# Kernel tuning notes

Hardware: AMD Instinct MI355X
Metric: run time of the kernel (lower is better)

## Reference

```python
import jax, jax.numpy as jnp
import numpy as np


def _conv(x, w, b):
    # PyTorch Conv2d(k=4, s=2, p=1): NCHW x OIHW correlation
    y = jax.lax.conv_general_dilated(x, w, window_strides=(2, 2),
                                     padding=((1, 1), (1, 1)),
                                     dimension_numbers=('NCHW', 'OIHW', 'NCHW'))
    return y + b[None, :, None, None]


def _conv_t(x, w, b):
    # PyTorch ConvTranspose2d(k=4, s=2, p=1); w has torch shape (Cin, Cout, 4, 4).
    # Adjoint of strided correlation = correlation with spatially-flipped,
    # channel-swapped kernel and lhs dilation; pad = k - 1 - p = 2.
    wk = jnp.flip(w, (2, 3)).transpose(1, 0, 2, 3)  # (Cout, Cin, 4, 4)
    y = jax.lax.conv_general_dilated(x, wk, window_strides=(1, 1),
                                     padding=((2, 2), (2, 2)),
                                     lhs_dilation=(2, 2),
                                     dimension_numbers=('NCHW', 'OIHW', 'NCHW'))
    return y + b[None, :, None, None]


def setup_inputs() -> dict:
    key = jax.random.key(0)
    ks = jax.random.split(key, 18)
    s = 0.05
    inp = {'x': jax.random.normal(ks[0], (32, 3, 256, 256), jnp.float32)}
    # encoder weights (OIHW)
    enc_shapes = [(64, 3, 4, 4), (128, 64, 4, 4), (256, 128, 4, 4), (512, 256, 4, 4)]
    for i, sh in enumerate(enc_shapes):
        inp[f'e_w{i+1}'] = jax.random.normal(ks[1 + i], sh, jnp.float32) * s
        inp[f'e_b{i+1}'] = jnp.zeros((sh[0],), jnp.float32)
    # decoder weights (torch ConvTranspose2d layout: Cin, Cout, kH, kW)
    dec_shapes = [(512, 128, 4, 4), (128, 64, 4, 4), (64, 32, 4, 4), (32, 3, 4, 4)]
    for i, sh in enumerate(dec_shapes):
        inp[f'd_w{i+1}'] = jax.random.normal(ks[5 + i], sh, jnp.float32) * s
        inp[f'd_b{i+1}'] = jnp.zeros((sh[1],), jnp.float32)
    # codebook (num_embeddings=1024, embedding_dim=512)
    inp['embed'] = jax.random.normal(ks[9], (1024, 512), jnp.float32)
    return inp


def reference(x, e_w1, e_b1, e_w2, e_b2, e_w3, e_b3, e_w4, e_b4,
              d_w1, d_b1, d_w2, d_b2, d_w3, d_b3, d_w4, d_b4, embed):
    # encoder
    h = jax.nn.relu(_conv(x, e_w1, e_b1))
    h = jax.nn.relu(_conv(h, e_w2, e_b2))
    h = jax.nn.relu(_conv(h, e_w3, e_b3))
    z = jax.nn.relu(_conv(h, e_w4, e_b4))  # (B, 512, 16, 16)
    # quantizer: NCHW -> NHWC -> flat (B*H*W, D)
    B, D, H, W = z.shape
    z_flat = z.transpose(0, 2, 3, 1).reshape(-1, D)
    # squared L2 distance to each code: ||z||^2 - 2 z.E^T + ||E||^2
    dist = (jnp.sum(z_flat ** 2, axis=1, keepdims=True)
            - 2.0 * z_flat @ embed.T
            + jnp.sum(embed ** 2, axis=1))  # (N, K)
    idx = jnp.argmin(dist, axis=1)
    quantized = embed[idx]  # gather == one_hot @ embed
    z_q = quantized.reshape(B, H, W, D).transpose(0, 3, 1, 2)  # NCHW
    # decoder
    h = jax.nn.relu(_conv_t(z_q, d_w1, d_b1))
    h = jax.nn.relu(_conv_t(h, d_w2, d_b2))
    h = jax.nn.relu(_conv_t(h, d_w3, d_b3))
    out = jnp.tanh(_conv_t(h, d_w4, d_b4))  # (B, 3, 256, 256)
    return out
```

## Files before the change

kernel.cpp:

```cpp
#include <hip/hip_runtime.h>
#include <math.h>


typedef __attribute__((ext_vector_type(8))) short bf16x8;
typedef __attribute__((ext_vector_type(4))) float f32x4;
union FragU { unsigned u[4]; bf16x8 v; };

__device__ __forceinline__ unsigned bf16_rne(unsigned u) {
    return (u + 0x7FFFu + ((u >> 16) & 1u)) >> 16;
}
__device__ __forceinline__ unsigned pack_split(float v) {
    unsigned u = __builtin_bit_cast(unsigned, v);
    unsigned hi = bf16_rne(u);
    float hif = __builtin_bit_cast(float, hi << 16);
    float r = v - hif;
    unsigned lo = bf16_rne(__builtin_bit_cast(unsigned, r));
    return hi | (lo << 16);
}

__global__ void __launch_bounds__(256) pack_tensor(
    const float* __restrict__ s, unsigned* __restrict__ d, int n)
{
    int i = blockIdx.x * 256 + threadIdx.x;
    if (i < n) d[i] = pack_split(s[i]);
}

__global__ void __launch_bounds__(256) pack_w1(
    const float* __restrict__ w, unsigned* __restrict__ wq)
{
    int idx = blockIdx.x * 256 + threadIdx.x;
    if (idx >= 64 * 64) return;
    int k = idx & 63, oc = idx >> 6;
    float v = (k < 48) ? w[oc * 48 + k] : 0.0f;
    wq[idx] = pack_split(v);
}

template<int Cout, int K>
__global__ void __launch_bounds__(256) pack_w_planes(
    const float* __restrict__ w, unsigned* __restrict__ wq)
{
    constexpr int K2 = K / 2;
    constexpr int TOT = Cout * K;
    int idx = blockIdx.x * 256 + threadIdx.x;
    if (idx >= TOT) return;
    int kp   = idx % K2;
    int rest = idx / K2;
    int oc   = rest % Cout;
    int p    = rest / Cout;
    unsigned u0 = pack_split(w[(size_t)oc * K + 2 * kp]);
    unsigned u1 = pack_split(w[(size_t)oc * K + 2 * kp + 1]);
    wq[idx] = (p == 0) ? ((u0 & 0xffffu) | (u1 << 16))
                       : ((u0 >> 16) | (u1 & 0xffff0000u));
}

template<int Cin, int Cout>
__global__ void __launch_bounds__(256) repack_wt_planes(
    const float* __restrict__ w, unsigned* __restrict__ wq)
{
    constexpr int K = Cin * 4, K2 = K / 2;
    constexpr int TOT = 2 * 4 * Cout * K2;
    int idx = blockIdx.x * 256 + threadIdx.x;
    if (idx >= TOT) return;
    int kp   = idx % K2;
    int rest = idx / K2;
    int co   = rest % Cout;
    rest    /= Cout;
    int par  = rest & 3;
    int p    = rest >> 2;
    int dy = par >> 1, dx = par & 1;
    unsigned u01[2];
#pragma unroll
    for (int e = 0; e < 2; ++e) {
        int k = 2 * kp + e;
        int t = k & 3, ci = k >> 2;
        int r = t >> 1, s = t & 1;
        int ky = 3 - dy - 2 * r;
        int kx = 3 - dx - 2 * s;
        u01[e] = pack_split(w[(((size_t)ci * Cout + co) * 4 + ky) * 4 + kx]);
    }
    wq[idx] = (p == 0) ? ((u01[0] & 0xffffu) | (u01[1] << 16))
                       : ((u01[0] >> 16) | (u01[1] & 0xffff0000u));
}

__global__ void __launch_bounds__(256) embed_transpose(
    const float* __restrict__ embed, float* __restrict__ et)
{
    int idx = blockIdx.x * 256 + threadIdx.x;
    int c = idx & 1023, k = idx >> 10;
    et[idx] = embed[(size_t)c * 512 + k];
}

template<int Cin, int H, int W, int Cout, int NB, int PACKO>
__global__ void __launch_bounds__(256) conv4s2_mfma(
    const unsigned* __restrict__ xp, const unsigned* __restrict__ wp,
    const float* __restrict__ bias, float* __restrict__ y)
{
    constexpr int OH = H / 2, OW = W / 2;
    constexpr int LOG_OW = (OW == 64) ? 6 : (OW == 32) ? 5 : 4;
    constexpr int R   = 64 / OW;
    constexpr int RT  = 2 * R + 2;
    constexpr int CS  = W + 2;
    constexpr int CS2 = CS + 2;
    constexpr int XEL = 2 * RT * CS;
    constexpr int XIT = (XEL + 255) / 256;
    constexpr int K   = Cin * 16;
    constexpr int K2  = K / 2;
    constexpr int NC  = Cin / 2;
    constexpr int NT  = NB / 64;
    constexpr int WR  = NB / 16;
    constexpr int WIT = NB / 8;
    constexpr int MBC = 32 * OH * OW / 64;
    constexpr int RAWU = RT * CS2;
    constexpr int OFF_RL = RAWU;
    constexpr int OFF_WH = ((2 * RAWU) + 7) & ~7;
    constexpr int OFF_WL = OFF_WH + NB * 20;
    constexpr int SM1 = OFF_WL + NB * 20;
    constexpr int SM2 = NB * 68;
    constexpr int SMEM = SM1 > SM2 ? SM1 : SM2;

    __shared__ unsigned smem[SMEM];
    unsigned short* rawh = (unsigned short*)smem;
    unsigned short* rawl = (unsigned short*)(smem + OFF_RL);
    unsigned* wbh = smem + OFF_WH;
    unsigned* wbl = smem + OFF_WL;

    int bid = blockIdx.x;
    int mb = bid % MBC, ng = bid / MBC;
    int oc0 = ng * NB;
    int m0 = mb * 64;
    int nimg = m0 / (OH * OW);
    int sp0 = m0 % (OH * OW);
    int oyb = sp0 >> LOG_OW;

    int tid  = threadIdx.x;
    int lane = tid & 63, wv = tid >> 6;
    int lm = lane & 15, q = lane >> 4;
    int n0w = wv * 16 * NT;

    const unsigned* xbase = xp + (size_t)nimg * Cin * H * W;

    int  goff[XIT];
    bool gok[XIT];
    int  sidx[XIT];
#pragma unroll
    for (int s = 0; s < XIT; ++s) {
        int i = tid + 256 * s;
        goff[s] = 0; gok[s] = false; sidx[s] = 0;
        if (i < XEL) {
            int lc = i % CS;
            int t2 = i / CS;
            int lr = t2 % RT;
            int c  = t2 / RT;
            int gr = 2 * oyb - 1 + lr;
            int gc = lc - 1;
            bool ok = ((unsigned)gr < (unsigned)H) && ((unsigned)gc < (unsigned)W);
            goff[s] = ok ? (c * H * W + gr * W + gc) : 0;
            gok[s]  = ok;
            sidx[s] = (c * RT + lr) * CS2 + lc;
        }
    }
    const unsigned* wbase_h = wp + (size_t)(oc0 + (tid >> 4)) * K2 + (tid & 15);
    const unsigned* wbase_l = wbase_h + (size_t)Cout * K2;
    int wlds0 = (tid >> 4) * 20 + (tid & 15);

    f32x4 acc[4][NT];
#pragma unroll
    for (int nt = 0; nt < NT; ++nt) {
        float b = bias[oc0 + n0w + nt * 16 + lm];
#pragma unroll
        for (int mt = 0; mt < 4; ++mt)
#pragma unroll
            for (int r = 0; r < 4; ++r) acc[mt][nt][r] = b;
    }

    unsigned pfa[XIT];
    unsigned pfb[WIT];

    auto load_chunk = [&](int ch) {
        const unsigned* cb = xbase + (size_t)(ch * 2) * (H * W);
#pragma unroll
        for (int s = 0; s < XIT; ++s) {
            unsigned v = 0;
            if (gok[s]) v = cb[goff[s]];
            pfa[s] = v;
        }
        const unsigned* wch = wbase_h + ch * 16;
        const unsigned* wcl = wbase_l + ch * 16;
#pragma unroll
        for (int s = 0; s < WR; ++s) {
            pfb[2 * s]     = wch[(size_t)s * 16 * K2];
            pfb[2 * s + 1] = wcl[(size_t)s * 16 * K2];
        }
    };
    auto store_chunk = [&]() {
#pragma unroll
        for (int s = 0; s < XIT; ++s) {
            int i = tid + 256 * s;
            if (i < XEL) {
                rawh[sidx[s]] = (unsigned short)(pfa[s] & 0xffffu);
                rawl[sidx[s]] = (unsigned short)(pfa[s] >> 16);
            }
        }
#pragma unroll
        for (int s = 0; s < WR; ++s) {
            wbh[wlds0 + s * 16 * 20] = pfb[2 * s];
            wbl[wlds0 + s * 16 * 20] = pfb[2 * s + 1];
        }
    };

    load_chunk(0);
#pragma unroll 1
    for (int ch = 0; ch < NC; ++ch) {
        __syncthreads();
        store_chunk();
        __syncthreads();
        if (ch + 1 < NC) load_chunk(ch + 1);

        FragU bhi[NT], blo[NT];
#pragma unroll
        for (int nt = 0; nt < NT; ++nt) {
            int oc = n0w + nt * 16 + lm;
            uint4 th = *(const uint4*)&wbh[oc * 20 + q * 4];
            uint4 tl = *(const uint4*)&wbl[oc * 20 + q * 4];
            bhi[nt].u[0] = th.x; bhi[nt].u[1] = th.y;
            bhi[nt].u[2] = th.z; bhi[nt].u[3] = th.w;
            blo[nt].u[0] = tl.x; blo[nt].u[1] = tl.y;
            blo[nt].u[2] = tl.z; blo[nt].u[3] = tl.w;
        }
#pragma unroll
        for (int mt = 0; mt < 4; ++mt) {
            int m = mt * 16 + lm;
            int oyl = m >> LOG_OW, oxl = m & (OW - 1);
            int c = q >> 1, rb = 2 * oyl + (q & 1) * 2;
            int bidx = (c * RT + rb) * CS2 + 2 * oxl;
            FragU ahi, alo;
            ahi.u[0] = *(const unsigned*)&rawh[bidx];
            ahi.u[1] = *(const unsigned*)&rawh[bidx + 2];
            ahi.u[2] = *(const unsigned*)&rawh[bidx + CS2];
            ahi.u[3] = *(const unsigned*)&rawh[bidx + CS2 + 2];
            alo.u[0] = *(const unsigned*)&rawl[bidx];
            alo.u[1] = *(const unsigned*)&rawl[bidx + 2];
            alo.u[2] = *(const unsigned*)&rawl[bidx + CS2];
            alo.u[3] = *(const unsigned*)&rawl[bidx + CS2 + 2];
#pragma unroll
            for (int nt = 0; nt < NT; ++nt) {
                acc[mt][nt] = __builtin_amdgcn_mfma_f32_16x16x32_bf16(
                    ahi.v, bhi[nt].v, acc[mt][nt], 0, 0, 0);
                acc[mt][nt] = __builtin_amdgcn_mfma_f32_16x16x32_bf16(
                    ahi.v, blo[nt].v, acc[mt][nt], 0, 0, 0);
                acc[mt][nt] = __builtin_amdgcn_mfma_f32_16x16x32_bf16(
                    alo.v, bhi[nt].v, acc[mt][nt], 0, 0, 0);
            }
        }
    }

    __syncthreads();
    float* cs = (float*)smem;
#pragma unroll
    for (int mt = 0; mt < 4; ++mt)
#pragma unroll
        for (int nt = 0; nt < NT; ++nt) {
            int nl = n0w + nt * 16 + lm;
#pragma unroll
            for (int r = 0; r < 4; ++r)
                cs[nl * 68 + mt * 16 + q * 4 + r] = acc[mt][nt][r];
        }
    __syncthreads();
    {
        constexpr int QT = 256 / NB;
        constexpr int MQ = 64 / QT;
        int nl = tid / QT, qt = tid % QT;
        size_t gb = ((size_t)(nimg * Cout + oc0 + nl)) * (OH * OW) + sp0 + qt * MQ;
#pragma unroll
        for (int i2 = 0; i2 < MQ / 4; ++i2) {
            float4 v = *(float4*)&cs[nl * 68 + qt * MQ + 4 * i2];
            v.x = fmaxf(v.x, 0.0f); v.y = fmaxf(v.y, 0.0f);
            v.z = fmaxf(v.z, 0.0f); v.w = fmaxf(v.w, 0.0f);
            if (PACKO) {
                uint4 p;
                p.x = pack_split(v.x); p.y = pack_split(v.y);
                p.z = pack_split(v.z); p.w = pack_split(v.w);
                *(uint4*)((unsigned*)y + gb + 4 * i2) = p;
            } else {
                *(float4*)(y + gb + 4 * i2) = v;
            }
        }
    }
}

template<int Cin, int CINR, int H, int W, int Cout, int MT, int NT, int PACKO>
__global__ void __launch_bounds__(256) conv4s2_mfma_g(
    const unsigned* __restrict__ xp, const unsigned* __restrict__ wp,
    const float* __restrict__ bias, float* __restrict__ y)
{
    constexpr int OH = H / 2, OW = W / 2;
    constexpr int OWB = (OW >= 64) ? 64 : OW;
    constexpr int LOG_OWB = (OWB == 64) ? 6 : (OWB == 32) ? 5 : 4;
    constexpr int LOG_OW  = (OW == 128) ? 7 : (OW == 64) ? 6 : (OW == 32) ? 5 : 4;
    constexpr int R   = 64 / OWB;
    constexpr int RT  = 2 * R + 2;
    constexpr int CS  = 2 * OWB + 2;
    constexpr int XEL = 2 * RT * CS;
    constexpr int XIT = (XEL + 255) / 256;
    constexpr int K   = Cin * 16;
    constexpr int NC  = Cin / 2;
    constexpr int NB  = Cout;
    constexpr int WIT = NB / 8;
    constexpr int WN  = Cout / (16 * NT);
    constexpr int WM  = 4 / WN;
    static_assert(WM * MT * 16 == 64, "M tiling");
    static_assert(WN * NT * 16 == Cout, "N tiling");
    constexpr int MBC = 32 * OH * OW / 64;
    constexpr int XPAD = (XEL + 7) & ~7;
    constexpr int SM1 = XPAD + NB * 36;
    constexpr int SM2 = NB * 68;
    constexpr int SMEM = SM1 > SM2 ? SM1 : SM2;

    __shared__ unsigned smem[SMEM];
    unsigned* raw = smem;
    unsigned* wb  = smem + XPAD;

    int bid = blockIdx.x;
    int mb = bid % MBC, ng = bid / MBC;
    int oc0 = ng * NB;
    int m0 = mb * 64;
    int nimg = m0 / (OH * OW);
    int sp0 = m0 % (OH * OW);
    int oyb = sp0 >> LOG_OW;
    int oxb = sp0 & (OW - 1);

    int tid  = threadIdx.x;
    int lane = tid & 63, wv = tid >> 6;
    int lm = lane & 15, q = lane >> 4;
    int wm = wv / WN, wn = wv % WN;

    const unsigned* xbase = xp + (size_t)nimg * CINR * H * W;

    int  goff[XIT];
    bool gok[XIT];
    int  cidx[XIT];
#pragma unroll
    for (int s = 0; s < XIT; ++s) {
        int i = tid + 256 * s;
        goff[s] = 0; gok[s] = false; cidx[s] = 0;
        if (i < XEL) {
            int lc = i % CS;
            int t2 = i / CS;
            int lr = t2 % RT;
            int c  = t2 / RT;
            int gr = 2 * oyb - 1 + lr;
            int gc = 2 * oxb - 1 + lc;
            bool ok = ((unsigned)gr < (unsigned)H) && ((unsigned)gc < (unsigned)W);
            goff[s] = ok ? (c * H * W + gr * W + gc) : 0;
            gok[s]  = ok;
            cidx[s] = c;
        }
    }
    const unsigned* wbase = wp + (size_t)(oc0 + (tid >> 5)) * K + (tid & 31);
    int wlds0 = (tid >> 5) * 36 + (tid & 31);

    f32x4 acc[MT][NT];
#pragma unroll
    for (int nt = 0; nt < NT; ++nt) {
        float b = bias[oc0 + wn * NT * 16 + nt * 16 + lm];
#pragma unroll
        for (int mt = 0; mt < MT; ++mt)
#pragma unroll
            for (int r = 0; r < 4; ++r) acc[mt][nt][r] = b;
    }

    unsigned pfa[XIT];
    unsigned pfb[WIT];

    auto load_chunk = [&](int ch) {
        const unsigned* cb = xbase + (size_t)(ch * 2) * (H * W);
#pragma unroll
        for (int s = 0; s < XIT; ++s) {
            unsigned v = 0;
            bool okc = (2 * ch + cidx[s]) < CINR;
            if (gok[s] && okc) v = cb[goff[s]];
            pfa[s] = v;
        }
        const unsigned* wc = wbase + ch * 32;
#pragma unroll
        for (int s = 0; s < WIT; ++s) pfb[s] = wc[(size_t)s * 8 * K];
    };
    auto store_chunk = [&]() {
#pragma unroll
        for (int s = 0; s < XIT; ++s) {
            int i = tid + 256 * s;
            if (i < XEL) raw[i] = pfa[s];
        }
#pragma unroll
        for (int s = 0; s < WIT; ++s) wb[wlds0 + s * 288] = pfb[s];
    };

    load_chunk(0);
#pragma unroll 1
    for (int ch = 0; ch < NC; ++ch) {
        __syncthreads();
        store_chunk();
        __syncthreads();
        if (ch + 1 < NC) load_chunk(ch + 1);

        FragU bhi[NT], blo[NT];
#pragma unroll
        for (int nt = 0; nt < NT; ++nt) {
            const unsigned* bp = &wb[(wn * NT * 16 + nt * 16 + lm) * 36 + q * 8];
            uint4 p0 = *(const uint4*)bp;
            uint4 p1 = *(const uint4*)(bp + 4);
            unsigned e0 = p0.x, e1 = p0.y, e2 = p0.z, e3 = p0.w;
            unsigned e4 = p1.x, e5 = p1.y, e6 = p1.z, e7 = p1.w;
            bhi[nt].u[0] = (e0 & 0xffffu) | (e1 << 16);
            bhi[nt].u[1] = (e2 & 0xffffu) | (e3 << 16);
            bhi[nt].u[2] = (e4 & 0xffffu) | (e5 << 16);
            bhi[nt].u[3] = (e6 & 0xffffu) | (e7 << 16);
            blo[nt].u[0] = (e0 >> 16) | (e1 & 0xffff0000u);
            blo[nt].u[1] = (e2 >> 16) | (e3 & 0xffff0000u);
            blo[nt].u[2] = (e4 >> 16) | (e5 & 0xffff0000u);
            blo[nt].u[3] = (e6 >> 16) | (e7 & 0xffff0000u);
        }
#pragma unroll
        for (int mt = 0; mt < MT; ++mt) {
            int m = wm * (MT * 16) + mt * 16 + lm;
            int oyl = m >> LOG_OWB, oxl = m & (OWB - 1);
            int c = q >> 1, rb = 2 * oyl + (q & 1) * 2;
            const unsigned* rp = &raw[(c * RT + rb) * CS + 2 * oxl];
            uint2 a0 = *(const uint2*)rp;
            uint2 a1 = *(const uint2*)(rp + 2);
            uint2 a2 = *(const uint2*)(rp + CS);
            uint2 a3 = *(const uint2*)(rp + CS + 2);
            FragU ahi, alo;
            ahi.u[0] = (a0.x & 0xffffu) | (a0.y << 16);
            ahi.u[1] = (a1.x & 0xffffu) | (a1.y << 16);
            ahi.u[2] = (a2.x & 0xffffu) | (a2.y << 16);
            ahi.u[3] = (a3.x & 0xffffu) | (a3.y << 16);
            alo.u[0] = (a0.x >> 16) | (a0.y & 0xffff0000u);
            alo.u[1] = (a1.x >> 16) | (a1.y & 0xffff0000u);
            alo.u[2] = (a2.x >> 16) | (a2.y & 0xffff0000u);
            alo.u[3] = (a3.x >> 16) | (a3.y & 0xffff0000u);
#pragma unroll
            for (int nt = 0; nt < NT; ++nt) {
                acc[mt][nt] = __builtin_amdgcn_mfma_f32_16x16x32_bf16(
                    ahi.v, bhi[nt].v, acc[mt][nt], 0, 0, 0);
                acc[mt][nt] = __builtin_amdgcn_mfma_f32_16x16x32_bf16(
                    ahi.v, blo[nt].v, acc[mt][nt], 0, 0, 0);
                acc[mt][nt] = __builtin_amdgcn_mfma_f32_16x16x32_bf16(
                    alo.v, bhi[nt].v, acc[mt][nt], 0, 0, 0);
            }
        }
    }

    __syncthreads();
    float* cs = (float*)smem;
#pragma unroll
    for (int mt = 0; mt < MT; ++mt)
#pragma unroll
        for (int nt = 0; nt < NT; ++nt) {
            int nl  = wn * NT * 16 + nt * 16 + lm;
            int mb2 = wm * (MT * 16) + mt * 16 + q * 4;
#pragma unroll
            for (int r = 0; r < 4; ++r)
                cs[nl * 68 + mb2 + r] = acc[mt][nt][r];
        }
    __syncthreads();
    {
        constexpr int QT = 256 / NB;
        constexpr int MQ = 64 / QT;
        int nl = tid / QT, qt = tid % QT;
        size_t gb = ((size_t)(nimg * Cout + oc0 + nl)) * (OH * OW) + sp0 + qt * MQ;
#pragma unroll
        for (int i2 = 0; i2 < MQ / 4; ++i2) {
            float4 v = *(float4*)&cs[nl * 68 + qt * MQ + 4 * i2];
            v.x = fmaxf(v.x, 0.0f); v.y = fmaxf(v.y, 0.0f);
            v.z = fmaxf(v.z, 0.0f); v.w = fmaxf(v.w, 0.0f);
            if (PACKO) {
                uint4 p;
                p.x = pack_split(v.x); p.y = pack_split(v.y);
                p.z = pack_split(v.z); p.w = pack_split(v.w);
                *(uint4*)((unsigned*)y + gb + 4 * i2) = p;
            } else {
                *(float4*)(y + gb + 4 * i2) = v;
            }
        }
    }
}

template<int Cin, int Hh, int Wh, int Cout, int MT, int NT, int PACKO>
__global__ void __launch_bounds__(256) convt4s2_mfma(
    const unsigned* __restrict__ xp, const unsigned* __restrict__ wq,
    const float* __restrict__ bias, float* __restrict__ y)
{
    constexpr int W = Wh;
    constexpr int LOG_W = (W == 64) ? 6 : (W == 32) ? 5 : 4;
    constexpr int R   = 64 / W;
    constexpr int RT  = R + 1;
    constexpr int CS  = W + 2;
    constexpr int XEL = 8 * RT * CS;
    constexpr int XIT = (XEL + 255) / 256;
    constexpr int K   = Cin * 4;
    constexpr int K2  = K / 2;
    constexpr int NC  = Cin / 8;
    constexpr int NB  = Cout;
    constexpr int WR  = NB / 16;
    constexpr int WIT = NB / 8;
    constexpr int WN  = Cout / (16 * NT);
    constexpr int WM  = 4 / WN;
    static_assert(WM * MT * 16 == 64, "M tiling");
    static_assert(WN * NT * 16 == Cout, "N tiling");
    constexpr int MBC = 32 * Hh * W / 64;
    constexpr int XPAD = (XEL + 7) & ~7;
    constexpr int OFF_WH = XPAD;
    constexpr int OFF_WL = OFF_WH + NB * 20;
    constexpr int OFF_AH = OFF_WL + NB * 20;
    constexpr int OFF_AL = OFF_AH + 64 * 20;
    constexpr int SM1 = OFF_AL + 64 * 20;
    constexpr int SM2 = NB * 68;
    constexpr int SMEM = SM1 > SM2 ? SM1 : SM2;

    __shared__ unsigned smem[SMEM];
    unsigned* raw = smem;
    unsigned* wbh = smem + OFF_WH;
    unsigned* wbl = smem + OFF_WL;
    unsigned* afh = smem + OFF_AH;
    unsigned* afl = smem + OFF_AL;

    int bid = blockIdx.x;
    int mb  = bid % MBC;
    int par = bid / MBC;
    int dy = par >> 1, dx = par & 1;

    int m0   = mb * 64;
    int nimg = m0 / (Hh * W);
    int sp0  = m0 % (Hh * W);
    int il0  = sp0 >> LOG_W;

    int tid = threadIdx.x;
    int lane = tid & 63, wv = tid >> 6;
    int lm = lane & 15, q = lane >> 4;
    int wm = wv / WN, wn = wv % WN;

    const unsigned* xbase = xp + (size_t)nimg * Cin * Hh * W;

    int  goff[XIT];
    bool gok[XIT];
#pragma unroll
    for (int s = 0; s < XIT; ++s) {
        int i = tid + 256 * s;
        goff[s] = 0; gok[s] = false;
        if (i < XEL) {
            int lc = i % CS;
            int t2 = i / CS;
            int lr = t2 % RT;
            int c  = t2 / RT;
            int gr = il0 - 1 + dy + lr;
            int gc = lc - 1;
            bool ok = ((unsigned)gr < (unsigned)Hh) && ((unsigned)gc < (unsigned)W);
            goff[s] = ok ? (c * Hh * W + gr * W + gc) : 0;
            gok[s]  = ok;
        }
    }
    const unsigned* wbase_h = wq + (size_t)(par * Cout + (tid >> 4)) * K2 + (tid & 15);
    const unsigned* wbase_l = wbase_h + (size_t)4 * Cout * K2;
    int wlds0 = (tid >> 4) * 20 + (tid & 15);

    f32x4 acc[MT][NT];
#pragma unroll
    for (int nt = 0; nt < NT; ++nt) {
        float b = bias[wn * NT * 16 + nt * 16 + lm];
#pragma unroll
        for (int mt = 0; mt < MT; ++mt)
#pragma unroll
            for (int r = 0; r < 4; ++r) acc[mt][nt][r] = b;
    }

    unsigned pfa[XIT];
    unsigned pfb[WIT];

    auto load_chunk = [&](int ch) {
        const unsigned* cb = xbase + (size_t)(ch * 8) * (Hh * W);
#pragma unroll
        for (int s = 0; s < XIT; ++s) {
            unsigned v = 0;
            if (gok[s]) v = cb[goff[s]];
            pfa[s] = v;
        }
        const unsigned* wch = wbase_h + ch * 16;
        const unsigned* wcl = wbase_l + ch * 16;
#pragma unroll
        for (int s = 0; s < WR; ++s) {
            pfb[2 * s]     = wch[(size_t)s * 16 * K2];
            pfb[2 * s + 1] = wcl[(size_t)s * 16 * K2];
        }
    };
    auto store_chunk = [&]() {
#pragma unroll
        for (int s = 0; s < XIT; ++s) {
            int i = tid + 256 * s;
            if (i < XEL) raw[i] = pfa[s];
        }
#pragma unroll
        for (int s = 0; s < WR; ++s) {
            wbh[wlds0 + s * 16 * 20] = pfb[2 * s];
            wbl[wlds0 + s * 16 * 20] = pfb[2 * s + 1];
        }
    };

    load_chunk(0);
#pragma unroll 1
    for (int ch = 0; ch < NC; ++ch) {
        __syncthreads();
        store_chunk();
        __syncthreads();
        {
            int m = tid >> 2, blk = tid & 3;
            int il = m >> LOG_W, jl = m & (W - 1);
            unsigned h[4], l[4];
#pragma unroll
            for (int j = 0; j < 4; ++j) {
                int kp = blk * 4 + j;
                int cl = kp >> 1, r = kp & 1;
                int ro = (cl * RT + il + r) * CS + jl + dx;
                unsigned r0 = raw[ro], r1 = raw[ro + 1];
                h[j] = (r0 & 0xffffu) | (r1 << 16);
                l[j] = (r0 >> 16) | (r1 & 0xffff0000u);
            }
            uint4 vh; vh.x = h[0]; vh.y = h[1]; vh.z = h[2]; vh.w = h[3];
            uint4 vl; vl.x = l[0]; vl.y = l[1]; vl.z = l[2]; vl.w = l[3];
            *(uint4*)&afh[m * 20 + blk * 4] = vh;
            *(uint4*)&afl[m * 20 + blk * 4] = vl;
        }
        if (ch + 1 < NC) load_chunk(ch + 1);
        __syncthreads();

        FragU bhi[NT], blo[NT];
#pragma unroll
        for (int nt = 0; nt < NT; ++nt) {
            int oc = wn * NT * 16 + nt * 16 + lm;
            uint4 th = *(const uint4*)&wbh[oc * 20 + q * 4];
            uint4 tl = *(const uint4*)&wbl[oc * 20 + q * 4];
            bhi[nt].u[0] = th.x; bhi[nt].u[1] = th.y;
            bhi[nt].u[2] = th.z; bhi[nt].u[3] = th.w;
            blo[nt].u[0] = tl.x; blo[nt].u[1] = tl.y;
            blo[nt].u[2] = tl.z; blo[nt].u[3] = tl.w;
        }
#pragma unroll
        for (int mt = 0; mt < MT; ++mt) {
            int ml = wm * (MT * 16) + mt * 16 + lm;
            uint4 ah = *(const uint4*)&afh[ml * 20 + q * 4];
            uint4 al = *(const uint4*)&afl[ml * 20 + q * 4];
            FragU ahi, alo;
            ahi.u[0] = ah.x; ahi.u[1] = ah.y; ahi.u[2] = ah.z; ahi.u[3] = ah.w;
            alo.u[0] = al.x; alo.u[1] = al.y; alo.u[2] = al.z; alo.u[3] = al.w;
#pragma unroll
            for (int nt = 0; nt < NT; ++nt) {
                acc[mt][nt] = __builtin_amdgcn_mfma_f32_16x16x32_bf16(
                    ahi.v, bhi[nt].v, acc[mt][nt], 0, 0, 0);
                acc[mt][nt] = __builtin_amdgcn_mfma_f32_16x16x32_bf16(
                    ahi.v, blo[nt].v, acc[mt][nt], 0, 0, 0);
                acc[mt][nt] = __builtin_amdgcn_mfma_f32_16x16x32_bf16(
                    alo.v, bhi[nt].v, acc[mt][nt], 0, 0, 0);
            }
        }
    }

    __syncthreads();
    float* cs = (float*)smem;
#pragma unroll
    for (int mt = 0; mt < MT; ++mt)
#pragma unroll
        for (int nt = 0; nt < NT; ++nt) {
            int nl  = wn * NT * 16 + nt * 16 + lm;
            int mb2 = wm * (MT * 16) + mt * 16 + q * 4;
#pragma unroll
            for (int r = 0; r < 4; ++r)
                cs[nl * 68 + mb2 + r] = acc[mt][nt][r];
        }
    __syncthreads();
    constexpr int EIT = NB * 64 / 256;
#pragma unroll
    for (int it = 0; it < EIT; ++it) {
        int idx = tid + 256 * it;
        int c = idx >> 6, m = idx & 63;
        int il = m >> LOG_W, jl = m & (W - 1);
        int oy = 2 * (il0 + il) + dy;
        int ox = 2 * jl + dx;
        float v = fmaxf(cs[c * 68 + m], 0.0f);
        size_t go = (((size_t)(nimg * Cout + c)) * (2 * Hh) + oy) * (2 * W) + ox;
        if (PACKO) ((unsigned*)y)[go] = pack_split(v);
        else       y[go] = v;
    }
}

template<int Cin, int H, int W, int Cout, int COT, int ACT, int UNR>
__global__ void __launch_bounds__(256) convt4s2_k(
    const float* __restrict__ x, const float* __restrict__ w,
    const float* __restrict__ bias, float* __restrict__ y)
{
    constexpr int OH = 2 * H, OW = 2 * W, OWq = OW / 4;
    int id = blockIdx.x * 256 + threadIdx.x;
    int ox4 = id % OWq; int t = id / OWq;
    int oy  = t % OH;   t /= OH;
    int cog = t % (Cout / COT);
    int n   = t / (Cout / COT);
    int co0 = __builtin_amdgcn_readfirstlane(cog * COT);
    n       = __builtin_amdgcn_readfirstlane(n);

    int p   = (oy + 1) & 1;
    int iyA = (oy + 1 - p) >> 1;
    int iyB = iyA - 1;
    bool vA = (iyA < H);
    bool vB = (iyB >= 0);
    int iyAc = vA ? iyA : 0, iyBc = vB ? iyB : 0;

    int t0 = 2 * ox4;
    bool c0 = (t0 - 1 >= 0);
    bool c3 = (t0 + 2 <= W - 1);
    int j0 = c0 ? t0 - 1 : 0;
    int j3 = c3 ? t0 + 2 : 0;

    float acc[COT][4];
#pragma unroll
    for (int o = 0; o < COT; ++o) {
        float b = bias[co0 + o];
#pragma unroll
        for (int j = 0; j < 4; ++j) acc[o][j] = b;
    }

    const float* xn = x + (size_t)n * Cin * H * W;

#pragma unroll UNR
    for (int ci = 0; ci < Cin; ++ci) {
        const float* xc  = xn + (size_t)ci * (H * W);
        const float* xrA = xc + (size_t)iyAc * W;
        const float* xrB = xc + (size_t)iyBc * W;
        float a0 = (vA && c0) ? xrA[j0]     : 0.0f;
        float a1 =  vA        ? xrA[t0]     : 0.0f;
        float a2 =  vA        ? xrA[t0 + 1] : 0.0f;
        float a3 = (vA && c3) ? xrA[j3]     : 0.0f;
        float b0 = (vB && c0) ? xrB[j0]     : 0.0f;
        float b1 =  vB        ? xrB[t0]     : 0.0f;
        float b2 =  vB        ? xrB[t0 + 1] : 0.0f;
        float b3 = (vB && c3) ? xrB[j3]     : 0.0f;

        const float* wci = w + ((size_t)ci * Cout + co0) * 16;
#pragma unroll
        for (int o = 0; o < COT; ++o) {
            const float* wr = wci + (size_t)o * 16;
            float wA0 = wr[p * 4 + 0], wA1 = wr[p * 4 + 1];
            float wA2 = wr[p * 4 + 2], wA3 = wr[p * 4 + 3];
            float wB0 = wr[(p + 2) * 4 + 0], wB1 = wr[(p + 2) * 4 + 1];
            float wB2 = wr[(p + 2) * 4 + 2], wB3 = wr[(p + 2) * 4 + 3];
            acc[o][0] = fmaf(a1, wA1, acc[o][0]); acc[o][0] = fmaf(a0, wA3, acc[o][0]);
            acc[o][0] = fmaf(b1, wB1, acc[o][0]); acc[o][0] = fmaf(b0, wB3, acc[o][0]);
            acc[o][1] = fmaf(a2, wA0, acc[o][1]); acc[o][1] = fmaf(a1, wA2, acc[o][1]);
            acc[o][1] = fmaf(b2, wB0, acc[o][1]); acc[o][1] = fmaf(b1, wB2, acc[o][1]);
            acc[o][2] = fmaf(a2, wA1, acc[o][2]); acc[o][2] = fmaf(a1, wA3, acc[o][2]);
            acc[o][2] = fmaf(b2, wB1, acc[o][2]); acc[o][2] = fmaf(b1, wB3, acc[o][2]);
            acc[o][3] = fmaf(a3, wA0, acc[o][3]); acc[o][3] = fmaf(a2, wA2, acc[o][3]);
            acc[o][3] = fmaf(b3, wB0, acc[o][3]); acc[o][3] = fmaf(b2, wB2, acc[o][3]);
        }
    }

    int ox0 = ox4 * 4;
#pragma unroll
    for (int o = 0; o < COT; ++o) {
        float* yr = y + (((size_t)n * Cout + co0 + o) * OH + oy) * OW + ox0;
#pragma unroll
        for (int j = 0; j < 4; ++j) {
            float v = acc[o][j];
            yr[j] = (ACT == 0) ? fmaxf(v, 0.0f) : tanhf(v);
        }
    }
}

__global__ void __launch_bounds__(256) embed_norms(
    const float* __restrict__ embed, float* __restrict__ norms)
{
    int c = blockIdx.x * 256 + threadIdx.x;
    const float* e = embed + (size_t)c * 512;
    float s = 0.0f;
    for (int k = 0; k < 512; ++k) s = fmaf(e[k], e[k], s);
    norms[c] = s;
}

__global__ void __launch_bounds__(256, 4) vq_argmin8v(
    const float* __restrict__ z, const float* __restrict__ et,
    const float* __restrict__ norms, int* __restrict__ out)
{
    constexpr int ZS = 516;
    int row0 = blockIdx.x * 8;
    int n    = row0 >> 8;
    int yx0  = row0 & 255;
    int tid  = threadIdx.x;

    __shared__ float zr[8 * ZS];

    const float* zn = z + ((size_t)n * 512) * 256;
#pragma unroll
    for (int it = 0; it < 4; ++it) {
        int i  = tid + 256 * it;
        int rq = i & 1, kc = i >> 1;
        float4 v = *(const float4*)&zn[(size_t)kc * 256 + yx0 + 4 * rq];
        zr[(4 * rq + 0) * ZS + kc] = v.x;
        zr[(4 * rq + 1) * ZS + kc] = v.y;
        zr[(4 * rq + 2) * ZS + kc] = v.z;
        zr[(4 * rq + 3) * ZS + kc] = v.w;
    }
    __syncthreads();

    f32x4 acc[8];
#pragma unroll
    for (int r = 0; r < 8; ++r) acc[r] = (f32x4){0.f, 0.f, 0.f, 0.f};

    const float* ebase = et + 4 * tid;
    f32x4 ev[4], fv[4];
#pragma unroll
    for (int j = 0; j < 4; ++j)
        ev[j] = *(const f32x4*)&ebase[(size_t)j * 1024];

#pragma unroll 1
    for (int k4 = 0; k4 < 128; ++k4) {
        int kn = (k4 + 1 < 128) ? k4 + 1 : 127;
#pragma unroll
        for (int j = 0; j < 4; ++j)
            fv[j] = *(const f32x4*)&ebase[(size_t)(4 * kn + j) * 1024];
#pragma unroll
        for (int r = 0; r < 8; ++r) {
            float4 zz = *(const float4*)&zr[r * ZS + 4 * k4];
            f32x4 a = acc[r];
            a += ev[0] * zz.x;
            a += ev[1] * zz.y;
            a += ev[2] * zz.z;
            a += ev[3] * zz.w;
            acc[r] = a;
        }
#pragma unroll
        for (int j = 0; j < 4; ++j) ev[j] = fv[j];
    }

    float4 nb = *(const float4*)&norms[4 * tid];
    float best[8]; int bi[8];
#pragma unroll
    for (int r = 0; r < 8; ++r) {
        float d0 = nb.x - 2.0f * acc[r][0];
        float d1 = nb.y - 2.0f * acc[r][1];
        float d2 = nb.z - 2.0f * acc[r][2];
        float d3 = nb.w - 2.0f * acc[r][3];
        float b = d0; int ix = 4 * tid;
        if (d1 < b) { b = d1; ix = 4 * tid + 1; }
        if (d2 < b) { b = d2; ix = 4 * tid + 2; }
        if (d3 < b) { b = d3; ix = 4 * tid + 3; }
        best[r] = b; bi[r] = ix;
    }

    __syncthreads();
    float* rbd = zr;
    int*   rbi = (int*)(zr + 2048);
#pragma unroll
    for (int r = 0; r < 8; ++r) {
        rbd[r * 256 + tid] = best[r];
        rbi[r * 256 + tid] = bi[r];
    }
    __syncthreads();
    for (int s = 128; s > 0; s >>= 1) {
        if (tid < s) {
#pragma unroll
            for (int r = 0; r < 8; ++r) {
                int i0 = r * 256 + tid;
                float od = rbd[i0 + s]; int oi = rbi[i0 + s];
                float md = rbd[i0];     int mi = rbi[i0];
                if (od < md || (od == md && oi < mi)) { rbd[i0] = od; rbi[i0] = oi; }
            }
        }
        __syncthreads();
    }
    if (tid < 8) out[row0 + tid] = rbi[tid * 256];
}

__global__ void __launch_bounds__(256) vq_gather_pack(
    const int* __restrict__ vidx, const float* __restrict__ embed,
    unsigned* __restrict__ zq)
{
    int i = blockIdx.x * 256 + threadIdx.x;
    int yx = i & 255;
    int t  = i >> 8;
    int c  = t & 511;
    int n  = t >> 9;
    int row = (n << 8) + yx;
    zq[i] = pack_split(embed[(size_t)vidx[row] * 512 + c]);
}

extern "C" void kernel_launch(void* const* d_in, const int* in_sizes, int n_in,
                              void* d_out, int out_size, void* d_ws, size_t ws_size,
                              hipStream_t stream)
{
    (void)in_sizes; (void)n_in; (void)out_size; (void)ws_size;
    const float* x     = (const float*)d_in[0];
    const float* ew1   = (const float*)d_in[1];
    const float* eb1   = (const float*)d_in[2];
    const float* ew2   = (const float*)d_in[3];
    const float* eb2   = (const float*)d_in[4];
    const float* ew3   = (const float*)d_in[5];
    const float* eb3   = (const float*)d_in[6];
    const float* ew4   = (const float*)d_in[7];
    const float* eb4   = (const float*)d_in[8];
    const float* dw1   = (const float*)d_in[9];
    const float* db1   = (const float*)d_in[10];
    const float* dw2   = (const float*)d_in[11];
    const float* db2   = (const float*)d_in[12];
    const float* dw3   = (const float*)d_in[13];
    const float* db3   = (const float*)d_in[14];
    const float* dw4   = (const float*)d_in[15];
    const float* db4   = (const float*)d_in[16];
    const float* embed = (const float*)d_in[17];
    float* out = (float*)d_out;

    unsigned* W0   = (unsigned*)d_ws;
    unsigned* h1p  = W0;
    unsigned* h2p  = W0 + 33554432;
    unsigned* xp1  = W0 + 33554432;
    unsigned* h3p  = W0;
    float*    z    = (float*)(W0 + 8388608);
    unsigned* zq   = W0 + 12582912;
    float*    P0   = (float*)(W0 + 16777216);
    float*    P1   = (float*)(W0 + 20971520);
    int*      vidx = (int*)(W0 + 29360128);
    float*    norms= (float*)(W0 + 29368320);
    float*    g3o  = (float*)h2p;

    unsigned* wp2 = (unsigned*)d_out;
    unsigned* wp3 = wp2 + 131072;
    unsigned* wp4 = wp2 + 655360;
    unsigned* wq1 = wp2 + 2752512;
    unsigned* wq2 = wq1 + 1048576;
    unsigned* wq3 = wq2 + 131072;
    float*    et  = (float*)(wq3 + 32768);
    unsigned* wp1 = (unsigned*)(et + 524288);

    dim3 b256(256);

    pack_w_planes<128, 1024><<<dim3(512),  b256, 0, stream>>>(ew2, wp2);
    pack_w_planes<256, 2048><<<dim3(2048), b256, 0, stream>>>(ew3, wp3);
    pack_w_planes<512, 4096><<<dim3(8192), b256, 0, stream>>>(ew4, wp4);
    pack_w1<<<dim3(16), b256, 0, stream>>>(ew1, wp1);
    pack_tensor<<<dim3(24576), b256, 0, stream>>>(x, xp1, 6291456);
    repack_wt_planes<512, 128><<<dim3(4096), b256, 0, stream>>>(dw1, wq1);
    repack_wt_planes<128,  64><<<dim3(512),  b256, 0, stream>>>(dw2, wq2);
    repack_wt_planes< 64,  32><<<dim3(128),  b256, 0, stream>>>(dw3, wq3);
    embed_transpose<<<dim3(2048), b256, 0, stream>>>(embed, et);

    conv4s2_mfma_g<4, 3, 256, 256, 64, 4, 1, 1><<<dim3(8192), b256, 0, stream>>>(
        xp1, wp1, eb1, (float*)h1p);
    conv4s2_mfma<64, 128, 128, 128, 128, 1><<<dim3(2048), b256, 0, stream>>>(
        h1p, wp2, eb2, (float*)h2p);
    conv4s2_mfma<128, 64, 64, 256, 128, 1><<<dim3(1024), b256, 0, stream>>>(
        h2p, wp3, eb3, (float*)h3p);
    conv4s2_mfma<256, 32, 32, 512, 64, 0><<<dim3(1024), b256, 0, stream>>>(
        h3p, wp4, eb4, z);

    embed_norms<<<dim3(4), b256, 0, stream>>>(embed, norms);
    vq_argmin8v<<<dim3(1024), b256, 0, stream>>>(z, et, norms, vidx);
    vq_gather_pack<<<dim3(16384), b256, 0, stream>>>(vidx, embed, zq);

    convt4s2_mfma<512, 16, 16, 128, 4, 2, 1><<<dim3(4 * 128), b256, 0, stream>>>(
        zq, wq1, db1, P0);
    convt4s2_mfma<128, 32, 32, 64, 4, 1, 1><<<dim3(4 * 512), b256, 0, stream>>>(
        (const unsigned*)P0, wq2, db2, P1);
    convt4s2_mfma<64, 64, 64, 32, 2, 1, 0><<<dim3(4 * 2048), b256, 0, stream>>>(
        (const unsigned*)P1, wq3, db3, g3o);
    convt4s2_k<32, 128, 128, 3, 3, 1, 2><<<dim3(2048), b256, 0, stream>>>(
        g3o, dw4, db4, out);
}
```

Before: 1.130 ms.

## Double-buffer activation prefetch and halve epilogue LDS staging in conv kernel

The main loop of the conv kernel is unrolled by two and now keeps two register prefetch buffers for the input chunks. Activation loads run two chunks ahead of compute, while weight loads stay one chunk ahead, so global latency has more time to hide behind the MFMAs. The epilogue now stages the accumulator through a half-size LDS buffer in two passes, which shrinks the shared-memory maximum and may improve occupancy. The cost is more registers, which could lower occupancy, and extra barriers in the epilogue. The loop also assumes NC is even.

```diff
diff --git a/kernel.cpp b/kernel.cpp
--- a/kernel.cpp
+++ b/kernel.cpp
@@ -115,7 +115,7 @@
     constexpr int OFF_WH = ((2 * RAWU) + 7) & ~7;
     constexpr int OFF_WL = OFF_WH + NB * 20;
     constexpr int SM1 = OFF_WL + NB * 20;
-    constexpr int SM2 = NB * 68;
+    constexpr int SM2 = NB * 36;
     constexpr int SMEM = SM1 > SM2 ? SM1 : SM2;
 
     __shared__ unsigned smem[SMEM];
@@ -173,10 +173,10 @@
             for (int r = 0; r < 4; ++r) acc[mt][nt][r] = b;
     }
 
-    unsigned pfa[XIT];
+    unsigned pfa0[XIT], pfa1[XIT];
     unsigned pfb[WIT];
 
-    auto load_chunk = [&](int ch) {
+    auto load_a = [&](int ch, unsigned (&pfa)[XIT]) {
         const unsigned* cb = xbase + (size_t)(ch * 2) * (H * W);
 #pragma unroll
         for (int s = 0; s < XIT; ++s) {
@@ -184,6 +184,8 @@
             if (gok[s]) v = cb[goff[s]];
             pfa[s] = v;
         }
+    };
+    auto load_b = [&](int ch) {
         const unsigned* wch = wbase_h + ch * 16;
         const unsigned* wcl = wbase_l + ch * 16;
 #pragma unroll
@@ -192,7 +194,7 @@
             pfb[2 * s + 1] = wcl[(size_t)s * 16 * K2];
         }
     };
-    auto store_chunk = [&]() {
+    auto store_chunk = [&](unsigned (&pfa)[XIT]) {
 #pragma unroll
         for (int s = 0; s < XIT; ++s) {
             int i = tid + 256 * s;
@@ -207,15 +209,7 @@
             wbl[wlds0 + s * 16 * 20] = pfb[2 * s + 1];
         }
     };
-
-    load_chunk(0);
-#pragma unroll 1
-    for (int ch = 0; ch < NC; ++ch) {
-        __syncthreads();
-        store_chunk();
-        __syncthreads();
-        if (ch + 1 < NC) load_chunk(ch + 1);
-
+    auto compute = [&]() {
         FragU bhi[NT], blo[NT];
 #pragma unroll
         for (int nt = 0; nt < NT; ++nt) {
@@ -252,35 +246,58 @@
                     alo.v, bhi[nt].v, acc[mt][nt], 0, 0, 0);
             }
         }
-    }
-
-    __syncthreads();
+    };
+
+    load_a(0, pfa0);
+    load_b(0);
+    load_a(1, pfa1);
+#pragma unroll 1
+    for (int ch = 0; ch < NC; ch += 2) {
+        __syncthreads();
+        store_chunk(pfa0);
+        __syncthreads();
+        load_b(ch + 1);
+        if (ch + 2 < NC) load_a(ch + 2, pfa0);
+        compute();
+        __syncthreads();
+        store_chunk(pfa1);
+        __syncthreads();
+        if (ch + 2 < NC) load_b(ch + 2);
+        if (ch + 3 < NC) load_a(ch + 3, pfa1);
+        compute();
+    }
+
     float* cs = (float*)smem;
-#pragma unroll
-    for (int mt = 0; mt < 4; ++mt)
-#pragma unroll
-        for (int nt = 0; nt < NT; ++nt) {
-            int nl = n0w + nt * 16 + lm;
-#pragma unroll
-            for (int r = 0; r < 4; ++r)
-                cs[nl * 68 + mt * 16 + q * 4 + r] = acc[mt][nt][r];
-        }
-    __syncthreads();
-    {
-        constexpr int QT = 256 / NB;
-        constexpr int MQ = 64 / QT;
-        int nl = tid / QT, qt = tid % QT;
-        size_t gb = ((size_t)(nimg * Cout + oc0 + nl)) * (OH * OW) + sp0 + qt * MQ;
-#pragma unroll
-        for (int i2 = 0; i2 < MQ / 4; ++i2) {
-            float4 v = *(float4*)&cs[nl * 68 + qt * MQ + 4 * i2];
+    constexpr int QT = 256 / NB;
+    constexpr int MH = 32 / QT;
+    int nl = tid / QT, qt = tid % QT;
+#pragma unroll
+    for (int p = 0; p < 2; ++p) {
+        __syncthreads();
+#pragma unroll
+        for (int mh = 0; mh < 2; ++mh) {
+            int mt = 2 * p + mh;
+#pragma unroll
+            for (int nt = 0; nt < NT; ++nt) {
+                int nn = n0w + nt * 16 + lm;
+#pragma unroll
+                for (int r = 0; r < 4; ++r)
+                    cs[nn * 36 + mh * 16 + q * 4 + r] = acc[mt][nt][r];
+            }
+        }
+        __syncthreads();
+        size_t gb = ((size_t)(nimg * Cout + oc0 + nl)) * (OH * OW)
+                  + sp0 + p * 32 + qt * MH;
+#pragma unroll
+        for (int i2 = 0; i2 < MH / 4; ++i2) {
+            float4 v = *(float4*)&cs[nl * 36 + qt * MH + 4 * i2];
             v.x = fmaxf(v.x, 0.0f); v.y = fmaxf(v.y, 0.0f);
             v.z = fmaxf(v.z, 0.0f); v.w = fmaxf(v.w, 0.0f);
             if (PACKO) {
-                uint4 p;
-                p.x = pack_split(v.x); p.y = pack_split(v.y);
-                p.z = pack_split(v.z); p.w = pack_split(v.w);
-                *(uint4*)((unsigned*)y + gb + 4 * i2) = p;
+                uint4 pk;
+                pk.x = pack_split(v.x); pk.y = pack_split(v.y);
+                pk.z = pack_split(v.z); pk.w = pack_split(v.w);
+                *(uint4*)((unsigned*)y + gb + 4 * i2) = pk;
             } else {
                 *(float4*)(y + gb + 4 * i2) = v;
             }
```

Result: slower. 1.205 ms (+6.7%).

## Store interleaved hi/lo words in LDS and split planes at fragment load

Applied to the files above, without the earlier changes.

The encoder conv kernel now keeps activations and weights as packed 32-bit hi|lo words in shared memory, not as separate hi and lo 16-bit planes. The hi and lo bf16 fragments are rebuilt with mask/shift/or after vectorized LDS reads. This removes the scattered 16-bit LDS stores, the sidx index registers and the separate weight-plane packing kernels, which are replaced by the plain pack_tensor. In exchange, the inner loop does more ALU work per fragment, and the LDS weight reads are wider.

```diff
diff --git a/kernel.cpp b/kernel.cpp
--- a/kernel.cpp
+++ b/kernel.cpp
@@ -33,24 +33,6 @@
     int k = idx & 63, oc = idx >> 6;
     float v = (k < 48) ? w[oc * 48 + k] : 0.0f;
     wq[idx] = pack_split(v);
-}
-
-template<int Cout, int K>
-__global__ void __launch_bounds__(256) pack_w_planes(
-    const float* __restrict__ w, unsigned* __restrict__ wq)
-{
-    constexpr int K2 = K / 2;
-    constexpr int TOT = Cout * K;
-    int idx = blockIdx.x * 256 + threadIdx.x;
-    if (idx >= TOT) return;
-    int kp   = idx % K2;
-    int rest = idx / K2;
-    int oc   = rest % Cout;
-    int p    = rest / Cout;
-    unsigned u0 = pack_split(w[(size_t)oc * K + 2 * kp]);
-    unsigned u1 = pack_split(w[(size_t)oc * K + 2 * kp + 1]);
-    wq[idx] = (p == 0) ? ((u0 & 0xffffu) | (u1 << 16))
-                       : ((u0 >> 16) | (u1 & 0xffff0000u));
 }
 
 template<int Cin, int Cout>
@@ -100,29 +82,21 @@
     constexpr int R   = 64 / OW;
     constexpr int RT  = 2 * R + 2;
     constexpr int CS  = W + 2;
-    constexpr int CS2 = CS + 2;
     constexpr int XEL = 2 * RT * CS;
     constexpr int XIT = (XEL + 255) / 256;
     constexpr int K   = Cin * 16;
-    constexpr int K2  = K / 2;
     constexpr int NC  = Cin / 2;
     constexpr int NT  = NB / 64;
-    constexpr int WR  = NB / 16;
     constexpr int WIT = NB / 8;
     constexpr int MBC = 32 * OH * OW / 64;
-    constexpr int RAWU = RT * CS2;
-    constexpr int OFF_RL = RAWU;
-    constexpr int OFF_WH = ((2 * RAWU) + 7) & ~7;
-    constexpr int OFF_WL = OFF_WH + NB * 20;
-    constexpr int SM1 = OFF_WL + NB * 20;
+    constexpr int XPAD = (XEL + 7) & ~7;
+    constexpr int SM1 = XPAD + NB * 36;
     constexpr int SM2 = NB * 68;
     constexpr int SMEM = SM1 > SM2 ? SM1 : SM2;
 
     __shared__ unsigned smem[SMEM];
-    unsigned short* rawh = (unsigned short*)smem;
-    unsigned short* rawl = (unsigned short*)(smem + OFF_RL);
-    unsigned* wbh = smem + OFF_WH;
-    unsigned* wbl = smem + OFF_WL;
+    unsigned* raw = smem;
+    unsigned* wb  = smem + XPAD;
 
     int bid = blockIdx.x;
     int mb = bid % MBC, ng = bid / MBC;
@@ -141,11 +115,10 @@
 
     int  goff[XIT];
     bool gok[XIT];
-    int  sidx[XIT];
 #pragma unroll
     for (int s = 0; s < XIT; ++s) {
         int i = tid + 256 * s;
-        goff[s] = 0; gok[s] = false; sidx[s] = 0;
+        goff[s] = 0; gok[s] = false;
         if (i < XEL) {
             int lc = i % CS;
             int t2 = i / CS;
@@ -156,12 +129,10 @@
             bool ok = ((unsigned)gr < (unsigned)H) && ((unsigned)gc < (unsigned)W);
             goff[s] = ok ? (c * H * W + gr * W + gc) : 0;
             gok[s]  = ok;
-            sidx[s] = (c * RT + lr) * CS2 + lc;
-        }
-    }
-    const unsigned* wbase_h = wp + (size_t)(oc0 + (tid >> 4)) * K2 + (tid & 15);
-    const unsigned* wbase_l = wbase_h + (size_t)Cout * K2;
-    int wlds0 = (tid >> 4) * 20 + (tid & 15);
+        }
+    }
+    const unsigned* wbase = wp + (size_t)(oc0 + (tid >> 5)) * K + (tid & 31);
+    int wlds0 = (tid >> 5) * 36 + (tid & 31);
 
     f32x4 acc[4][NT];
 #pragma unroll
@@ -184,28 +155,18 @@
             if (gok[s]) v = cb[goff[s]];
             pfa[s] = v;
         }
-        const unsigned* wch = wbase_h + ch * 16;
-        const unsigned* wcl = wbase_l + ch * 16;
-#pragma unroll
-        for (int s = 0; s < WR; ++s) {
-            pfb[2 * s]     = wch[(size_t)s * 16 * K2];
-            pfb[2 * s + 1] = wcl[(size_t)s * 16 * K2];
-        }
+        const unsigned* wc = wbase + ch * 32;
+#pragma unroll
+        for (int s = 0; s < WIT; ++s) pfb[s] = wc[(size_t)s * 8 * K];
     };
     auto store_chunk = [&]() {
 #pragma unroll
         for (int s = 0; s < XIT; ++s) {
             int i = tid + 256 * s;
-            if (i < XEL) {
-                rawh[sidx[s]] = (unsigned short)(pfa[s] & 0xffffu);
-                rawl[sidx[s]] = (unsigned short)(pfa[s] >> 16);
-            }
-        }
-#pragma unroll
-        for (int s = 0; s < WR; ++s) {
-            wbh[wlds0 + s * 16 * 20] = pfb[2 * s];
-            wbl[wlds0 + s * 16 * 20] = pfb[2 * s + 1];
-        }
+            if (i < XEL) raw[i] = pfa[s];
+        }
+#pragma unroll
+        for (int s = 0; s < WIT; ++s) wb[wlds0 + s * 288] = pfb[s];
     };
 
     load_chunk(0);
@@ -219,29 +180,39 @@
         FragU bhi[NT], blo[NT];
 #pragma unroll
         for (int nt = 0; nt < NT; ++nt) {
-            int oc = n0w + nt * 16 + lm;
-            uint4 th = *(const uint4*)&wbh[oc * 20 + q * 4];
-            uint4 tl = *(const uint4*)&wbl[oc * 20 + q * 4];
-            bhi[nt].u[0] = th.x; bhi[nt].u[1] = th.y;
-            bhi[nt].u[2] = th.z; bhi[nt].u[3] = th.w;
-            blo[nt].u[0] = tl.x; blo[nt].u[1] = tl.y;
-            blo[nt].u[2] = tl.z; blo[nt].u[3] = tl.w;
+            const unsigned* bp = &wb[(n0w + nt * 16 + lm) * 36 + q * 8];
+            uint4 p0 = *(const uint4*)bp;
+            uint4 p1 = *(const uint4*)(bp + 4);
+            unsigned e0 = p0.x, e1 = p0.y, e2 = p0.z, e3 = p0.w;
+            unsigned e4 = p1.x, e5 = p1.y, e6 = p1.z, e7 = p1.w;
+            bhi[nt].u[0] = (e0 & 0xffffu) | (e1 << 16);
+            bhi[nt].u[1] = (e2 & 0xffffu) | (e3 << 16);
+            bhi[nt].u[2] = (e4 & 0xffffu) | (e5 << 16);
+            bhi[nt].u[3] = (e6 & 0xffffu) | (e7 << 16);
+            blo[nt].u[0] = (e0 >> 16) | (e1 & 0xffff0000u);
+            blo[nt].u[1] = (e2 >> 16) | (e3 & 0xffff0000u);
+            blo[nt].u[2] = (e4 >> 16) | (e5 & 0xffff0000u);
+            blo[nt].u[3] = (e6 >> 16) | (e7 & 0xffff0000u);
         }
 #pragma unroll
         for (int mt = 0; mt < 4; ++mt) {
             int m = mt * 16 + lm;
             int oyl = m >> LOG_OW, oxl = m & (OW - 1);
             int c = q >> 1, rb = 2 * oyl + (q & 1) * 2;
-            int bidx = (c * RT + rb) * CS2 + 2 * oxl;
+            const unsigned* rp = &raw[(c * RT + rb) * CS + 2 * oxl];
+            uint2 a0 = *(const uint2*)rp;
+            uint2 a1 = *(const uint2*)(rp + 2);
+            uint2 a2 = *(const uint2*)(rp + CS);
+            uint2 a3 = *(const uint2*)(rp + CS + 2);
             FragU ahi, alo;
-            ahi.u[0] = *(const unsigned*)&rawh[bidx];
-            ahi.u[1] = *(const unsigned*)&rawh[bidx + 2];
-            ahi.u[2] = *(const unsigned*)&rawh[bidx + CS2];
-            ahi.u[3] = *(const unsigned*)&rawh[bidx + CS2 + 2];
-            alo.u[0] = *(const unsigned*)&rawl[bidx];
-            alo.u[1] = *(const unsigned*)&rawl[bidx + 2];
-            alo.u[2] = *(const unsigned*)&rawl[bidx + CS2];
-            alo.u[3] = *(const unsigned*)&rawl[bidx + CS2 + 2];
+            ahi.u[0] = (a0.x & 0xffffu) | (a0.y << 16);
+            ahi.u[1] = (a1.x & 0xffffu) | (a1.y << 16);
+            ahi.u[2] = (a2.x & 0xffffu) | (a2.y << 16);
+            ahi.u[3] = (a3.x & 0xffffu) | (a3.y << 16);
+            alo.u[0] = (a0.x >> 16) | (a0.y & 0xffff0000u);
+            alo.u[1] = (a1.x >> 16) | (a1.y & 0xffff0000u);
+            alo.u[2] = (a2.x >> 16) | (a2.y & 0xffff0000u);
+            alo.u[3] = (a3.x >> 16) | (a3.y & 0xffff0000u);
 #pragma unroll
             for (int nt = 0; nt < NT; ++nt) {
                 acc[mt][nt] = __builtin_amdgcn_mfma_f32_16x16x32_bf16(
@@ -940,9 +911,9 @@
 
     dim3 b256(256);
 
-    pack_w_planes<128, 1024><<<dim3(512),  b256, 0, stream>>>(ew2, wp2);
-    pack_w_planes<256, 2048><<<dim3(2048), b256, 0, stream>>>(ew3, wp3);
-    pack_w_planes<512, 4096><<<dim3(8192), b256, 0, stream>>>(ew4, wp4);
+    pack_tensor<<<dim3(512),  b256, 0, stream>>>(ew2, wp2, 131072);
+    pack_tensor<<<dim3(2048), b256, 0, stream>>>(ew3, wp3, 524288);
+    pack_tensor<<<dim3(8192), b256, 0, stream>>>(ew4, wp4, 2097152);
     pack_w1<<<dim3(16), b256, 0, stream>>>(ew1, wp1);
     pack_tensor<<<dim3(24576), b256, 0, stream>>>(x, xp1, 6291456);
     repack_wt_planes<512, 128><<<dim3(4096), b256, 0, stream>>>(dw1, wq1);
```

Result: no change. 1.109 ms (-1.9%).
